# Optimization experiments

Measured on AMD Instinct MI355X. Metric: run time of the kernel, lower is better.

## Reference

```python
import jax, jax.numpy as jnp
import numpy as np

N_NODES = 50000
N_EDGES = 800000
IN_DIM = 128
HID = 32
OUT = 32
HEADS = 4
NEG_SLOPE = 0.2


def gat_conv(x, src, dst, W, al, ar, b, n_nodes):
    """DGL GATConv: x [N, F_in], W [F_in, H*D], al/ar [H, D], b [H*D].
    Returns [N, H, D]."""
    H, D = al.shape
    feat = (x @ W).reshape(-1, H, D)                     # [N, H, D]
    el = jnp.sum(feat * al, axis=-1)                     # [N, H]
    er = jnp.sum(feat * ar, axis=-1)                     # [N, H]
    e = jax.nn.leaky_relu(el[src] + er[dst], NEG_SLOPE)  # [E, H]
    # segment softmax over incoming edges of each destination
    m = jax.ops.segment_max(e, dst, num_segments=n_nodes)   # [N, H]
    ex = jnp.exp(e - m[dst])                                 # [E, H]
    denom = jax.ops.segment_sum(ex, dst, num_segments=n_nodes)  # [N, H]
    a = ex / denom[dst]                                      # [E, H]
    msg = feat[src] * a[:, :, None]                          # [E, H, D]
    out = jax.ops.segment_sum(msg, dst, num_segments=n_nodes)  # [N, H, D]
    return out + b.reshape(1, H, D)


def setup_inputs() -> dict:
    key = jax.random.key(0)
    ks = jax.random.split(key, 12)
    inputs = jax.random.normal(ks[0], (N_NODES, IN_DIM), dtype=jnp.float32)
    src = jax.random.randint(ks[1], (N_EDGES,), 0, N_NODES)
    dst = jax.random.randint(ks[2], (N_EDGES,), 0, N_NODES)
    s = 0.1
    W1 = jax.random.normal(ks[3], (IN_DIM, HEADS * HID), dtype=jnp.float32) * s
    al1 = jax.random.normal(ks[4], (HEADS, HID), dtype=jnp.float32) * s
    ar1 = jax.random.normal(ks[5], (HEADS, HID), dtype=jnp.float32) * s
    b1 = jnp.zeros((HEADS * HID,), dtype=jnp.float32)
    W2 = jax.random.normal(ks[6], (HEADS * HID, HEADS * OUT), dtype=jnp.float32) * s
    al2 = jax.random.normal(ks[7], (HEADS, OUT), dtype=jnp.float32) * s
    ar2 = jax.random.normal(ks[8], (HEADS, OUT), dtype=jnp.float32) * s
    b2 = jnp.zeros((HEADS * OUT,), dtype=jnp.float32)
    return {"inputs": inputs, "src": src, "dst": dst,
            "W1": W1, "al1": al1, "ar1": ar1, "b1": b1,
            "W2": W2, "al2": al2, "ar2": ar2, "b2": b2}


def reference(inputs, src, dst, W1, al1, ar1, b1, W2, al2, ar2, b2):
    n = inputs.shape[0]
    h = gat_conv(inputs, src, dst, W1, al1, ar1, b1, n)   # [N, H, HID]
    h = jax.nn.elu(h.reshape(n, -1))                      # flatten(1) + elu
    h = gat_conv(h, src, dst, W2, al2, ar2, b2, n)        # [N, H, OUT]
    return h.mean(axis=1)                                  # [N, OUT]
```

## Files before the change

### kernel.cpp

```cpp
#include <hip/hip_runtime.h>
#include <hip/hip_fp16.h>
#include <cmath>
#include <type_traits>

#define NEG_SLOPE 0.2f
#define BSHIFT 7
#define NBKMAX 512
#define BCAP   4096

typedef _Float16 f16x8 __attribute__((ext_vector_type(8)));
typedef float    f32x4 __attribute__((ext_vector_type(4)));

__device__ __forceinline__ int swz(int row, int kbyte) {
    return (row << 8) + (kbyte ^ ((row & 7) << 4));
}

__device__ __forceinline__ void scan512_excl(const int* __restrict__ g,
                                             int* sc, int* ws, int t) {
    int lane = t & 63, w = t >> 6;
    int a = g[2 * t], b = g[2 * t + 1];
    int ps = a + b;
    int x = ps;
#pragma unroll
    for (int off = 1; off < 64; off <<= 1) {
        int y = __shfl_up(x, off);
        if (lane >= off) x += y;
    }
    if (lane == 63) ws[w] = x;
    __syncthreads();
    int pre = 0;
#pragma unroll
    for (int i = 0; i < 4; ++i) pre += (i < w) ? ws[i] : 0;
    int e0 = pre + x - ps;
    sc[2 * t] = e0;
    sc[2 * t + 1] = e0 + a;
    __syncthreads();
}

__global__ __launch_bounds__(256) void transp(const float* __restrict__ W1,
                                              const float* __restrict__ W2,
                                              __half* __restrict__ Wt1,
                                              __half* __restrict__ Wt2,
                                              int* __restrict__ grel)
{
    int b = blockIdx.x;
    int t = threadIdx.x;
    if (b == 0) {
#pragma unroll
        for (int i = 0; i < 2; ++i) grel[t + 256 * i] = 0;
    }
    const float* W = (b < 4) ? W1 : W2;
    __half* Wt = (b < 4) ? Wt1 : Wt2;
    int q = b & 3;
#pragma unroll
    for (int i = 0; i < 4; ++i) {
        int idx = q * 1024 + t + 256 * i;
        int k = idx >> 5, nq = idx & 31;
        float4 v = ((const float4*)W)[idx];
        const float* vp = (const float*)&v;
#pragma unroll
        for (int j = 0; j < 4; ++j)
            Wt[(size_t)(nq * 4 + j) * 128 + k] = __float2half(vp[j]);
    }
}

template<typename AT>
__device__ __forceinline__ void gemm_body(char* lds,
                                          const AT* __restrict__ A,
                                          const __half* __restrict__ Wt,
                                          const float* __restrict__ al,
                                          const float* __restrict__ ar,
                                          __half* __restrict__ feat_h,
                                          float* __restrict__ el,
                                          float* __restrict__ er,
                                          int nrows, int bid)
{
    int t = threadIdx.x;
    int r0 = bid * 64;

#pragma unroll
    for (int i = 0; i < 4; ++i) {
        int cid = t + 256 * i;
        int row = cid >> 4, kc = cid & 15;
        int gr = r0 + row;
        f16x8 hv;
        if constexpr (std::is_same<AT, float>::value) {
            float4 v0 = make_float4(0, 0, 0, 0), v1 = v0;
            if (gr < nrows) {
                v0 = ((const float4*)A)[(size_t)gr * 32 + kc * 2];
                v1 = ((const float4*)A)[(size_t)gr * 32 + kc * 2 + 1];
            }
            hv[0] = (_Float16)v0.x; hv[1] = (_Float16)v0.y;
            hv[2] = (_Float16)v0.z; hv[3] = (_Float16)v0.w;
            hv[4] = (_Float16)v1.x; hv[5] = (_Float16)v1.y;
            hv[6] = (_Float16)v1.z; hv[7] = (_Float16)v1.w;
        } else {
            uint4 u = make_uint4(0, 0, 0, 0);
            if (gr < nrows) u = ((const uint4*)A)[(size_t)gr * 16 + kc];
            hv = *(const f16x8*)&u;
        }
        *(f16x8*)(lds + swz(row, kc * 16)) = hv;
    }
#pragma unroll
    for (int i = 0; i < 8; ++i) {
        int cid = t + 256 * i;
        int n = cid >> 4, kc = cid & 15;
        uint4 u = ((const uint4*)Wt)[(size_t)n * 16 + kc];
        *(uint4*)(lds + 16384 + swz(n, kc * 16)) = u;
    }
    __syncthreads();

    int w = t >> 6, lane = t & 63;
    int l15 = lane & 15, g = lane >> 4;

    f32x4 acc[8];
#pragma unroll
    for (int ct = 0; ct < 8; ++ct) acc[ct] = (f32x4){0.f, 0.f, 0.f, 0.f};

#pragma unroll
    for (int ks = 0; ks < 4; ++ks) {
        f16x8 a = *(const f16x8*)(lds + swz(w * 16 + l15, ks * 64 + g * 16));
#pragma unroll
        for (int ct = 0; ct < 8; ++ct) {
            f16x8 b = *(const f16x8*)(lds + 16384 + swz(ct * 16 + l15, ks * 64 + g * 16));
            acc[ct] = __builtin_amdgcn_mfma_f32_16x16x32_f16(a, b, acc[ct], 0, 0, 0);
        }
    }

#pragma unroll
    for (int j = 0; j < 4; ++j) {
        int gr = r0 + w * 16 + g * 4 + j;
        if (gr < nrows) {
#pragma unroll
            for (int ct = 0; ct < 8; ++ct)
                feat_h[(size_t)gr * 128 + ct * 16 + l15] = __float2half(acc[ct][j]);
        }
    }

    float alf[8], arf[8];
#pragma unroll
    for (int z = 0; z < 8; ++z) { alf[z] = al[z * 16 + l15]; arf[z] = ar[z * 16 + l15]; }
    float elv[4][4], erv[4][4];
#pragma unroll
    for (int j = 0; j < 4; ++j)
#pragma unroll
        for (int h = 0; h < 4; ++h) {
            elv[j][h] = acc[2*h][j] * alf[2*h] + acc[2*h+1][j] * alf[2*h+1];
            erv[j][h] = acc[2*h][j] * arf[2*h] + acc[2*h+1][j] * arf[2*h+1];
        }
#pragma unroll
    for (int off = 1; off < 16; off <<= 1) {
#pragma unroll
        for (int j = 0; j < 4; ++j)
#pragma unroll
            for (int h = 0; h < 4; ++h) {
                elv[j][h] += __shfl_xor(elv[j][h], off);
                erv[j][h] += __shfl_xor(erv[j][h], off);
            }
    }
    if (l15 == 0) {
#pragma unroll
        for (int j = 0; j < 4; ++j) {
            int gr = r0 + w * 16 + g * 4 + j;
            if (gr < nrows) {
#pragma unroll
                for (int h = 0; h < 4; ++h) {
                    el[gr * 4 + h] = elv[j][h];
                    er[gr * 4 + h] = erv[j][h];
                }
            }
        }
    }
}

__device__ __forceinline__ void part_a_body(char* smem,
                                            const int* __restrict__ src,
                                            const int* __restrict__ dst,
                                            int* __restrict__ grel,
                                            unsigned long long* __restrict__ ebuf,
                                            int ne, int nchunk, int bid)
{
    int* cnt   = (int*)smem;
    int* rbase = cnt + NBKMAX;
    int t = threadIdx.x;
    int c0 = bid * nchunk;
    int c1 = c0 + nchunk; if (c1 > ne) c1 = ne;
    for (int b = t; b < NBKMAX; b += 256) cnt[b] = 0;
    __syncthreads();
    for (int i = c0 + t; i < c1; i += 256)
        atomicAdd(&cnt[dst[i] >> BSHIFT], 1);
    __syncthreads();
    for (int b = t; b < NBKMAX; b += 256) {
        int c = cnt[b];
        rbase[b] = c ? atomicAdd(&grel[b], c) : 0;
        cnt[b] = 0;
    }
    __syncthreads();
    for (int i = c0 + t; i < c1; i += 256) {
        int d = dst[i];
        int b = d >> BSHIFT;
        int p = atomicAdd(&cnt[b], 1);
        int slot = rbase[b] + p;
        if (slot < BCAP)
            ebuf[(size_t)b * BCAP + slot] =
                ((unsigned long long)(unsigned)d << 32) | (unsigned)src[i];
    }
}

__global__ __launch_bounds__(256) void gemm1_parta(const float* __restrict__ X,
                                                   const __half* __restrict__ Wt1,
                                                   const float* __restrict__ al,
                                                   const float* __restrict__ ar,
                                                   __half* __restrict__ feat_h,
                                                   float* __restrict__ el,
                                                   float* __restrict__ er, int nrows,
                                                   const int* __restrict__ src,
                                                   const int* __restrict__ dst,
                                                   int* __restrict__ grel,
                                                   unsigned long long* __restrict__ ebuf,
                                                   int ne, int nchunk, int ngemm)
{
    __shared__ __align__(16) char smem[49152];
    int bid = blockIdx.x;
    if (bid < ngemm)
        gemm_body<float>(smem, X, Wt1, al, ar, feat_h, el, er, nrows, bid);
    else
        part_a_body(smem, src, dst, grel, ebuf, ne, nchunk, bid - ngemm);
}

__global__ __launch_bounds__(256) void gemm_mfma_h(const __half* __restrict__ A,
                                                   const __half* __restrict__ Wt,
                                                   const float* __restrict__ al,
                                                   const float* __restrict__ ar,
                                                   __half* __restrict__ feat_h,
                                                   float* __restrict__ el,
                                                   float* __restrict__ er, int nrows)
{
    __shared__ __align__(16) char smem[49152];
    gemm_body<__half>(smem, A, Wt, al, ar, feat_h, el, er, nrows, blockIdx.x);
}

__global__ __launch_bounds__(256) void part_b(const unsigned long long* __restrict__ ebuf,
                                              const int* __restrict__ grel,
                                              int* __restrict__ offs,
                                              int* __restrict__ ssrc,
                                              int nnodes, int ne)
{
    __shared__ int sc[NBKMAX];
    __shared__ int ws[4];
    __shared__ int hcnt[128];
    __shared__ int curs[128];
    __shared__ int w0tot;
    int b = blockIdx.x;
    int t = threadIdx.x;
    int lane = t & 63;
    scan512_excl(grel, sc, ws, t);
    int node0 = b << BSHIFT;
    int csrbase = sc[b];
    int count = grel[b]; if (count > BCAP) count = BCAP;
    const unsigned long long* eb = ebuf + (size_t)b * BCAP;
    if (t < 128) hcnt[t] = 0;
    __syncthreads();
    for (int i = t; i < count; i += 256) {
        int d = (int)(eb[i] >> 32);
        atomicAdd(&hcnt[d - node0], 1);
    }
    __syncthreads();
    int v = (t < 128) ? hcnt[t] : 0;
    int x = v;
#pragma unroll
    for (int off = 1; off < 64; off <<= 1) {
        int y = __shfl_up(x, off);
        if (lane >= off) x += y;
    }
    if (t == 63) w0tot = x;
    __syncthreads();
    if (t < 128) {
        int incl = x + ((t >= 64) ? w0tot : 0);
        int gpos = csrbase + incl - v;
        curs[t] = gpos;
        int node = node0 + t;
        if (node < nnodes) offs[node] = gpos;
    }
    if (b == 0 && t == 0) offs[nnodes] = ne;
    __syncthreads();
    for (int i = t; i < count; i += 256) {
        unsigned long long e = eb[i];
        int d = (int)(e >> 32);
        int p = atomicAdd(&curs[d - node0], 1);
        ssrc[p] = (int)(unsigned)(e & 0xffffffffu);
    }
}

template<int LAYER>
__global__ __launch_bounds__(256) void aggregate(const __half2* __restrict__ feat,
                                                 const float* __restrict__ el,
                                                 const float* __restrict__ er,
                                                 const int* __restrict__ offs,
                                                 const int* __restrict__ ssrc,
                                                 const float* __restrict__ bias,
                                                 void* __restrict__ out, int nnodes)
{
    __shared__ float w_sh[4][256];
    int wid  = threadIdx.x >> 6;
    int lane = threadIdx.x & 63;
    int gw = blockIdx.x * 4 + wid;
    if (gw >= nnodes) return;
    int beg = offs[gw], end = offs[gw + 1];
    float4 er4 = ((const float4*)er)[gw];
    const float4* el4 = (const float4*)el;
    int h = lane >> 4;

    float accx = 0.f, accy = 0.f;
    float d0 = 0.f, d1 = 0.f, d2 = 0.f, d3 = 0.f;

    for (int cbeg = beg; cbeg < end; cbeg += 64) {
        int cnt = end - cbeg; if (cnt > 64) cnt = 64;
        int myS = (lane < cnt) ? ssrc[cbeg + lane] : 0;
        float4 e4 = el4[myS];
        float ex0 = 0.f, ex1 = 0.f, ex2 = 0.f, ex3 = 0.f;
        if (lane < cnt) {
            float e;
            e = e4.x + er4.x; ex0 = __expf(fmaxf(e, 0.f) + NEG_SLOPE * fminf(e, 0.f));
            e = e4.y + er4.y; ex1 = __expf(fmaxf(e, 0.f) + NEG_SLOPE * fminf(e, 0.f));
            e = e4.z + er4.z; ex2 = __expf(fmaxf(e, 0.f) + NEG_SLOPE * fminf(e, 0.f));
            e = e4.w + er4.w; ex3 = __expf(fmaxf(e, 0.f) + NEG_SLOPE * fminf(e, 0.f));
            d0 += ex0; d1 += ex1; d2 += ex2; d3 += ex3;
        }
        ((float4*)&w_sh[wid][0])[lane] = make_float4(ex0, ex1, ex2, ex3);

#pragma unroll
        for (int g = 0; g < 4; ++g) {
            if (g * 16 < cnt) {
                __half2 f[16]; float w[16];
#pragma unroll
                for (int k = 0; k < 16; ++k) {
                    int s = __builtin_amdgcn_readlane(myS, g * 16 + k);
                    f[k] = feat[(size_t)s * 64 + lane];
                    w[k] = w_sh[wid][(g * 16 + k) * 4 + h];
                }
#pragma unroll
                for (int k = 0; k < 16; ++k) {
                    float2 ff = __half22float2(f[k]);
                    accx += ff.x * w[k];
                    accy += ff.y * w[k];
                }
            }
        }
    }

#pragma unroll
    for (int off = 32; off; off >>= 1) {
        d0 += __shfl_xor(d0, off);
        d1 += __shfl_xor(d1, off);
        d2 += __shfl_xor(d2, off);
        d3 += __shfl_xor(d3, off);
    }
    float dh   = h == 0 ? d0 : h == 1 ? d1 : h == 2 ? d2 : d3;
    float invh = dh > 0.f ? 1.f / dh : 0.f;
    accx *= invh; accy *= invh;

    int c = lane * 2;
    if (LAYER == 1) {
        float v0 = accx + bias[c];
        float v1 = accy + bias[c + 1];
        v0 = v0 > 0.f ? v0 : expm1f(v0);
        v1 = v1 > 0.f ? v1 : expm1f(v1);
        ((__half2*)out)[(size_t)gw * 64 + lane] = __floats2half2_rn(v0, v1);
    } else {
        float v0 = accx + bias[c];
        float v1 = accy + bias[c + 1];
        v0 += __shfl_xor(v0, 16); v0 += __shfl_xor(v0, 32);
        v1 += __shfl_xor(v1, 16); v1 += __shfl_xor(v1, 32);
        if (lane < 16)
            ((float2*)out)[(size_t)gw * 16 + lane] = make_float2(v0 * 0.25f, v1 * 0.25f);
    }
}

template __global__ void aggregate<1>(const __half2*, const float*, const float*,
                                      const int*, const int*, const float*, void*, int);
template __global__ void aggregate<2>(const __half2*, const float*, const float*,
                                      const int*, const int*, const float*, void*, int);

extern "C" void kernel_launch(void* const* d_in, const int* in_sizes, int n_in,
                              void* d_out, int out_size, void* d_ws, size_t ws_size,
                              hipStream_t stream)
{
    const float* X   = (const float*)d_in[0];
    const int*   src = (const int*)d_in[1];
    const int*   dst = (const int*)d_in[2];
    const float* W1  = (const float*)d_in[3];
    const float* al1 = (const float*)d_in[4];
    const float* ar1 = (const float*)d_in[5];
    const float* b1  = (const float*)d_in[6];
    const float* W2  = (const float*)d_in[7];
    const float* al2 = (const float*)d_in[8];
    const float* ar2 = (const float*)d_in[9];
    const float* b2  = (const float*)d_in[10];
    float* out = (float*)d_out;

    const int N = in_sizes[0] / 128;
    const int E = in_sizes[1];
    const int NBK = (N + 127) >> BSHIFT;
    const int NCH = (E + 255) / 256;
    const int NGEMM = (N + 63) / 64;

    size_t off = 0;
    char* base = (char*)d_ws;
    auto alloc = [&](size_t bytes) -> void* {
        void* p = base + off;
        off += (bytes + 255) & ~(size_t)255;
        return p;
    };
    __half* feat_h = (__half*)alloc((size_t)N * 128 * 2);
    __half* hbuf_h = (__half*)alloc((size_t)N * 128 * 2);
    float*  el     = (float*)alloc((size_t)N * 4 * 4);
    float*  er     = (float*)alloc((size_t)N * 4 * 4);
    int*    offs   = (int*)alloc((size_t)(N + 1) * 4);
    int*    ssrc   = (int*)alloc((size_t)E * 4);
    unsigned long long* ebuf = (unsigned long long*)alloc((size_t)NBKMAX * BCAP * 8);
    int*    grel   = (int*)alloc(NBKMAX * 4);
    __half* Wt1    = (__half*)alloc(128 * 128 * 2);
    __half* Wt2    = (__half*)alloc(128 * 128 * 2);
    (void)ws_size; (void)n_in; (void)out_size;

    transp<<<8, 256, 0, stream>>>(W1, W2, Wt1, Wt2, grel);

    gemm1_parta<<<NGEMM + 256, 256, 0, stream>>>(X, Wt1, al1, ar1, feat_h, el, er, N,
                                                 src, dst, grel, ebuf, E, NCH, NGEMM);

    part_b<<<NBK, 256, 0, stream>>>(ebuf, grel, offs, ssrc, N, E);

    aggregate<1><<<(N + 3) / 4, 256, 0, stream>>>((const __half2*)feat_h, el, er, offs, ssrc, b1, hbuf_h, N);

    gemm_mfma_h<<<NGEMM, 256, 0, stream>>>(hbuf_h, Wt2, al2, ar2, feat_h, el, er, N);

    aggregate<2><<<(N + 3) / 4, 256, 0, stream>>>((const __half2*)feat_h, el, er, offs, ssrc, b2, out, N);
}
```

Before: 130.1 us.

## Fuse bucket CSR build into aggregation kernels using per-block LDS sorting

Removes the separate CSR-building kernel and the global offs/ssrc arrays. Each aggregation block now sorts its own destination bucket of edges into LDS and aggregates those nodes directly. Buckets shrink to 64 nodes with a smaller capacity so the sorted source list fits in shared memory. The cost is that the bucket sort is redone in both layers, and each wave now processes 16 nodes serially, which greatly reduces the number of waves available to hide gather latency.

```diff
diff --git a/kernel.cpp b/kernel.cpp
--- a/kernel.cpp
+++ b/kernel.cpp
@@ -4,37 +4,15 @@
 #include <type_traits>
 
 #define NEG_SLOPE 0.2f
-#define BSHIFT 7
-#define NBKMAX 512
-#define BCAP   4096
+#define BSHIFT 6
+#define NBKMAX 1024
+#define BCAP   2048
 
 typedef _Float16 f16x8 __attribute__((ext_vector_type(8)));
 typedef float    f32x4 __attribute__((ext_vector_type(4)));
 
 __device__ __forceinline__ int swz(int row, int kbyte) {
     return (row << 8) + (kbyte ^ ((row & 7) << 4));
-}
-
-__device__ __forceinline__ void scan512_excl(const int* __restrict__ g,
-                                             int* sc, int* ws, int t) {
-    int lane = t & 63, w = t >> 6;
-    int a = g[2 * t], b = g[2 * t + 1];
-    int ps = a + b;
-    int x = ps;
-#pragma unroll
-    for (int off = 1; off < 64; off <<= 1) {
-        int y = __shfl_up(x, off);
-        if (lane >= off) x += y;
-    }
-    if (lane == 63) ws[w] = x;
-    __syncthreads();
-    int pre = 0;
-#pragma unroll
-    for (int i = 0; i < 4; ++i) pre += (i < w) ? ws[i] : 0;
-    int e0 = pre + x - ps;
-    sc[2 * t] = e0;
-    sc[2 * t + 1] = e0 + a;
-    __syncthreads();
 }
 
 __global__ __launch_bounds__(256) void transp(const float* __restrict__ W1,
@@ -47,7 +25,7 @@
     int t = threadIdx.x;
     if (b == 0) {
 #pragma unroll
-        for (int i = 0; i < 2; ++i) grel[t + 256 * i] = 0;
+        for (int i = 0; i < 4; ++i) grel[t + 256 * i] = 0;
     }
     const float* W = (b < 4) ? W1 : W2;
     __half* Wt = (b < 4) ? Wt1 : Wt2;
@@ -240,147 +218,139 @@
     gemm_body<__half>(smem, A, Wt, al, ar, feat_h, el, er, nrows, blockIdx.x);
 }
 
-__global__ __launch_bounds__(256) void part_b(const unsigned long long* __restrict__ ebuf,
-                                              const int* __restrict__ grel,
-                                              int* __restrict__ offs,
-                                              int* __restrict__ ssrc,
-                                              int nnodes, int ne)
-{
-    __shared__ int sc[NBKMAX];
-    __shared__ int ws[4];
-    __shared__ int hcnt[128];
-    __shared__ int curs[128];
-    __shared__ int w0tot;
+template<int LAYER>
+__global__ __launch_bounds__(256) void agg_bucket(const __half2* __restrict__ feat,
+                                                  const float* __restrict__ el,
+                                                  const float* __restrict__ er,
+                                                  const int* __restrict__ grel,
+                                                  const unsigned long long* __restrict__ ebuf,
+                                                  const float* __restrict__ bias,
+                                                  void* __restrict__ out, int nnodes)
+{
+    __shared__ int   hcnt[64];
+    __shared__ int   curs[64];
+    __shared__ int   loffs[65];
+    __shared__ int   lsrc[BCAP];
+    __shared__ float w_sh[4][256];
+
     int b = blockIdx.x;
     int t = threadIdx.x;
     int lane = t & 63;
-    scan512_excl(grel, sc, ws, t);
+    int wid  = t >> 6;
     int node0 = b << BSHIFT;
-    int csrbase = sc[b];
     int count = grel[b]; if (count > BCAP) count = BCAP;
     const unsigned long long* eb = ebuf + (size_t)b * BCAP;
-    if (t < 128) hcnt[t] = 0;
+
+    if (t < 64) hcnt[t] = 0;
     __syncthreads();
     for (int i = t; i < count; i += 256) {
         int d = (int)(eb[i] >> 32);
         atomicAdd(&hcnt[d - node0], 1);
     }
     __syncthreads();
-    int v = (t < 128) ? hcnt[t] : 0;
-    int x = v;
-#pragma unroll
-    for (int off = 1; off < 64; off <<= 1) {
-        int y = __shfl_up(x, off);
-        if (lane >= off) x += y;
-    }
-    if (t == 63) w0tot = x;
-    __syncthreads();
-    if (t < 128) {
-        int incl = x + ((t >= 64) ? w0tot : 0);
-        int gpos = csrbase + incl - v;
-        curs[t] = gpos;
-        int node = node0 + t;
-        if (node < nnodes) offs[node] = gpos;
-    }
-    if (b == 0 && t == 0) offs[nnodes] = ne;
+    if (wid == 0) {
+        int v = hcnt[lane];
+        int x = v;
+#pragma unroll
+        for (int off = 1; off < 64; off <<= 1) {
+            int y = __shfl_up(x, off);
+            if (lane >= off) x += y;
+        }
+        loffs[lane + 1] = x;
+        if (lane == 0) loffs[0] = 0;
+        curs[lane] = x - v;
+    }
     __syncthreads();
     for (int i = t; i < count; i += 256) {
         unsigned long long e = eb[i];
         int d = (int)(e >> 32);
         int p = atomicAdd(&curs[d - node0], 1);
-        ssrc[p] = (int)(unsigned)(e & 0xffffffffu);
-    }
-}
-
-template<int LAYER>
-__global__ __launch_bounds__(256) void aggregate(const __half2* __restrict__ feat,
-                                                 const float* __restrict__ el,
-                                                 const float* __restrict__ er,
-                                                 const int* __restrict__ offs,
-                                                 const int* __restrict__ ssrc,
-                                                 const float* __restrict__ bias,
-                                                 void* __restrict__ out, int nnodes)
-{
-    __shared__ float w_sh[4][256];
-    int wid  = threadIdx.x >> 6;
-    int lane = threadIdx.x & 63;
-    int gw = blockIdx.x * 4 + wid;
-    if (gw >= nnodes) return;
-    int beg = offs[gw], end = offs[gw + 1];
-    float4 er4 = ((const float4*)er)[gw];
+        lsrc[p] = (int)(unsigned)(e & 0xffffffffu);
+    }
+    __syncthreads();
+
     const float4* el4 = (const float4*)el;
     int h = lane >> 4;
-
-    float accx = 0.f, accy = 0.f;
-    float d0 = 0.f, d1 = 0.f, d2 = 0.f, d3 = 0.f;
-
-    for (int cbeg = beg; cbeg < end; cbeg += 64) {
-        int cnt = end - cbeg; if (cnt > 64) cnt = 64;
-        int myS = (lane < cnt) ? ssrc[cbeg + lane] : 0;
-        float4 e4 = el4[myS];
-        float ex0 = 0.f, ex1 = 0.f, ex2 = 0.f, ex3 = 0.f;
-        if (lane < cnt) {
-            float e;
-            e = e4.x + er4.x; ex0 = __expf(fmaxf(e, 0.f) + NEG_SLOPE * fminf(e, 0.f));
-            e = e4.y + er4.y; ex1 = __expf(fmaxf(e, 0.f) + NEG_SLOPE * fminf(e, 0.f));
-            e = e4.z + er4.z; ex2 = __expf(fmaxf(e, 0.f) + NEG_SLOPE * fminf(e, 0.f));
-            e = e4.w + er4.w; ex3 = __expf(fmaxf(e, 0.f) + NEG_SLOPE * fminf(e, 0.f));
-            d0 += ex0; d1 += ex1; d2 += ex2; d3 += ex3;
-        }
-        ((float4*)&w_sh[wid][0])[lane] = make_float4(ex0, ex1, ex2, ex3);
-
-#pragma unroll
-        for (int g = 0; g < 4; ++g) {
-            if (g * 16 < cnt) {
-                __half2 f[16]; float w[16];
-#pragma unroll
-                for (int k = 0; k < 16; ++k) {
-                    int s = __builtin_amdgcn_readlane(myS, g * 16 + k);
-                    f[k] = feat[(size_t)s * 64 + lane];
-                    w[k] = w_sh[wid][(g * 16 + k) * 4 + h];
-                }
-#pragma unroll
-                for (int k = 0; k < 16; ++k) {
-                    float2 ff = __half22float2(f[k]);
-                    accx += ff.x * w[k];
-                    accy += ff.y * w[k];
+    int c = lane * 2;
+
+    for (int ln = wid * 16; ln < wid * 16 + 16; ++ln) {
+        int node = node0 + ln;
+        if (node >= nnodes) break;
+        int beg = loffs[ln], end = loffs[ln + 1];
+        float4 er4 = ((const float4*)er)[node];
+
+        float accx = 0.f, accy = 0.f;
+        float d0 = 0.f, d1 = 0.f, d2 = 0.f, d3 = 0.f;
+
+        for (int cbeg = beg; cbeg < end; cbeg += 64) {
+            int cnt = end - cbeg; if (cnt > 64) cnt = 64;
+            int myS = (lane < cnt) ? lsrc[cbeg + lane] : 0;
+            float4 e4 = el4[myS];
+            float ex0 = 0.f, ex1 = 0.f, ex2 = 0.f, ex3 = 0.f;
+            if (lane < cnt) {
+                float e;
+                e = e4.x + er4.x; ex0 = __expf(fmaxf(e, 0.f) + NEG_SLOPE * fminf(e, 0.f));
+                e = e4.y + er4.y; ex1 = __expf(fmaxf(e, 0.f) + NEG_SLOPE * fminf(e, 0.f));
+                e = e4.z + er4.z; ex2 = __expf(fmaxf(e, 0.f) + NEG_SLOPE * fminf(e, 0.f));
+                e = e4.w + er4.w; ex3 = __expf(fmaxf(e, 0.f) + NEG_SLOPE * fminf(e, 0.f));
+                d0 += ex0; d1 += ex1; d2 += ex2; d3 += ex3;
+            }
+            ((float4*)&w_sh[wid][0])[lane] = make_float4(ex0, ex1, ex2, ex3);
+
+#pragma unroll
+            for (int g = 0; g < 4; ++g) {
+                if (g * 16 < cnt) {
+                    __half2 f[16]; float w[16];
+#pragma unroll
+                    for (int k = 0; k < 16; ++k) {
+                        int s = __builtin_amdgcn_readlane(myS, g * 16 + k);
+                        f[k] = feat[(size_t)s * 64 + lane];
+                        w[k] = w_sh[wid][(g * 16 + k) * 4 + h];
+                    }
+#pragma unroll
+                    for (int k = 0; k < 16; ++k) {
+                        float2 ff = __half22float2(f[k]);
+                        accx += ff.x * w[k];
+                        accy += ff.y * w[k];
+                    }
                 }
             }
         }
-    }
-
-#pragma unroll
-    for (int off = 32; off; off >>= 1) {
-        d0 += __shfl_xor(d0, off);
-        d1 += __shfl_xor(d1, off);
-        d2 += __shfl_xor(d2, off);
-        d3 += __shfl_xor(d3, off);
-    }
-    float dh   = h == 0 ? d0 : h == 1 ? d1 : h == 2 ? d2 : d3;
-    float invh = dh > 0.f ? 1.f / dh : 0.f;
-    accx *= invh; accy *= invh;
-
-    int c = lane * 2;
-    if (LAYER == 1) {
-        float v0 = accx + bias[c];
-        float v1 = accy + bias[c + 1];
-        v0 = v0 > 0.f ? v0 : expm1f(v0);
-        v1 = v1 > 0.f ? v1 : expm1f(v1);
-        ((__half2*)out)[(size_t)gw * 64 + lane] = __floats2half2_rn(v0, v1);
-    } else {
-        float v0 = accx + bias[c];
-        float v1 = accy + bias[c + 1];
-        v0 += __shfl_xor(v0, 16); v0 += __shfl_xor(v0, 32);
-        v1 += __shfl_xor(v1, 16); v1 += __shfl_xor(v1, 32);
-        if (lane < 16)
-            ((float2*)out)[(size_t)gw * 16 + lane] = make_float2(v0 * 0.25f, v1 * 0.25f);
-    }
-}
-
-template __global__ void aggregate<1>(const __half2*, const float*, const float*,
-                                      const int*, const int*, const float*, void*, int);
-template __global__ void aggregate<2>(const __half2*, const float*, const float*,
-                                      const int*, const int*, const float*, void*, int);
+
+#pragma unroll
+        for (int off = 32; off; off >>= 1) {
+            d0 += __shfl_xor(d0, off);
+            d1 += __shfl_xor(d1, off);
+            d2 += __shfl_xor(d2, off);
+            d3 += __shfl_xor(d3, off);
+        }
+        float dh   = h == 0 ? d0 : h == 1 ? d1 : h == 2 ? d2 : d3;
+        float invh = dh > 0.f ? 1.f / dh : 0.f;
+        accx *= invh; accy *= invh;
+
+        if (LAYER == 1) {
+            float v0 = accx + bias[c];
+            float v1 = accy + bias[c + 1];
+            v0 = v0 > 0.f ? v0 : expm1f(v0);
+            v1 = v1 > 0.f ? v1 : expm1f(v1);
+            ((__half2*)out)[(size_t)node * 64 + lane] = __floats2half2_rn(v0, v1);
+        } else {
+            float v0 = accx + bias[c];
+            float v1 = accy + bias[c + 1];
+            v0 += __shfl_xor(v0, 16); v0 += __shfl_xor(v0, 32);
+            v1 += __shfl_xor(v1, 16); v1 += __shfl_xor(v1, 32);
+            if (lane < 16)
+                ((float2*)out)[(size_t)node * 16 + lane] = make_float2(v0 * 0.25f, v1 * 0.25f);
+        }
+    }
+}
+
+template __global__ void agg_bucket<1>(const __half2*, const float*, const float*,
+                                       const int*, const unsigned long long*,
+                                       const float*, void*, int);
+template __global__ void agg_bucket<2>(const __half2*, const float*, const float*,
+                                       const int*, const unsigned long long*,
+                                       const float*, void*, int);
 
 extern "C" void kernel_launch(void* const* d_in, const int* in_sizes, int n_in,
                               void* d_out, int out_size, void* d_ws, size_t ws_size,
@@ -401,7 +371,7 @@
 
     const int N = in_sizes[0] / 128;
     const int E = in_sizes[1];
-    const int NBK = (N + 127) >> BSHIFT;
+    const int NBK = (N + 63) >> BSHIFT;
     const int NCH = (E + 255) / 256;
     const int NGEMM = (N + 63) / 64;
 
@@ -416,8 +386,6 @@
     __half* hbuf_h = (__half*)alloc((size_t)N * 128 * 2);
     float*  el     = (float*)alloc((size_t)N * 4 * 4);
     float*  er     = (float*)alloc((size_t)N * 4 * 4);
-    int*    offs   = (int*)alloc((size_t)(N + 1) * 4);
-    int*    ssrc   = (int*)alloc((size_t)E * 4);
     unsigned long long* ebuf = (unsigned long long*)alloc((size_t)NBKMAX * BCAP * 8);
     int*    grel   = (int*)alloc(NBKMAX * 4);
     __half* Wt1    = (__half*)alloc(128 * 128 * 2);
@@ -429,11 +397,9 @@
     gemm1_parta<<<NGEMM + 256, 256, 0, stream>>>(X, Wt1, al1, ar1, feat_h, el, er, N,
                                                  src, dst, grel, ebuf, E, NCH, NGEMM);
 
-    part_b<<<NBK, 256, 0, stream>>>(ebuf, grel, offs, ssrc, N, E);
-
-    aggregate<1><<<(N + 3) / 4, 256, 0, stream>>>((const __half2*)feat_h, el, er, offs, ssrc, b1, hbuf_h, N);
+    agg_bucket<1><<<NBK, 256, 0, stream>>>((const __half2*)feat_h, el, er, grel, ebuf, b1, hbuf_h, N);
 
     gemm_mfma_h<<<NGEMM, 256, 0, stream>>>(hbuf_h, Wt2, al2, ar2, feat_h, el, er, N);
 
-    aggregate<2><<<(N + 3) / 4, 256, 0, stream>>>((const __half2*)feat_h, el, er, offs, ssrc, b2, out, N);
-}
+    agg_bucket<2><<<NBK, 256, 0, stream>>>((const __half2*)feat_h, el, er, grel, ebuf, b2, out, N);
+}
```

Result: slower. 155.1 us (+19.3%).
